# Optimization experiments

Measured on AMD Instinct MI355X. Metric: run time of the kernel, lower is better.

The kernel has to match this reference:

```python
import jax, jax.numpy as jnp
import numpy as np

N, E, DIN, HID, DOUT = 50000, 800000, 128, 128, 64
NEG_SLOPE = 0.2


def setup_inputs() -> dict:
    key = jax.random.key(0)
    ks = jax.random.split(key, 16)
    x = jax.random.normal(ks[0], (N, DIN), dtype=jnp.float32)
    edge_index = jax.random.randint(ks[1], (2, E), 0, N, dtype=jnp.int64)

    def lin(k, fan_in, fan_out):
        kw, kb = jax.random.split(k)
        s = 1.0 / np.sqrt(fan_in)
        W = jax.random.uniform(kw, (fan_in, fan_out), jnp.float32, -s, s)
        b = jax.random.uniform(kb, (fan_out,), jnp.float32, -s, s)
        return W, b

    Wl, bl = lin(ks[2], DIN, DIN)   # GATv2 lin_l
    Wr, br = lin(ks[3], DIN, DIN)   # GATv2 lin_r
    att = jax.random.uniform(ks[4], (DIN,), jnp.float32, -1.0 / np.sqrt(DIN), 1.0 / np.sqrt(DIN))
    bg = jnp.zeros((DIN,), jnp.float32)  # GAT output bias
    W1, b1 = lin(ks[5], DIN, HID)   # ChebConv K=1 -> plain linear
    W2, b2 = lin(ks[6], HID, HID)
    W3, b3 = lin(ks[7], HID, DOUT)
    return {"x": x, "edge_index": edge_index, "Wl": Wl, "bl": bl, "Wr": Wr,
            "br": br, "att": att, "bg": bg, "W1": W1, "b1": b1,
            "W2": W2, "b2": b2, "W3": W3, "b3": b3}


def reference(x, edge_index, Wl, bl, Wr, br, att, bg, W1, b1, W2, b2, W3, b3):
    n = x.shape[0]
    # GATv2Conv adds self loops by default
    loop = jnp.arange(n, dtype=edge_index.dtype)
    src = jnp.concatenate([edge_index[0], loop])  # source j
    dst = jnp.concatenate([edge_index[1], loop])  # target i

    xl = x @ Wl + bl  # [N, DIN]
    xr = x @ Wr + br  # [N, DIN]

    # GATv2 edge scores: leaky_relu(x_l[j] + x_r[i]) . att
    e = jax.nn.leaky_relu(xl[src] + xr[dst], NEG_SLOPE)  # [E+N, DIN]
    a = e @ att                                          # [E+N]

    # softmax over incoming edges of each destination node
    amax = jax.ops.segment_max(a, dst, num_segments=n)
    ea = jnp.exp(a - amax[dst])
    denom = jax.ops.segment_sum(ea, dst, num_segments=n)
    alpha = ea / denom[dst]                              # [E+N]

    # aggregate messages alpha * x_l[j] at destinations
    h = jax.ops.segment_sum(alpha[:, None] * xl[src], dst, num_segments=n) + bg

    # ChebConv with K=1 reduces to a linear layer (T_0(L) = I)
    h = jax.nn.relu(h @ W1 + b1)
    h = jax.nn.relu(h @ W2 + b2)
    # dropout_rate = 0.0 -> identity
    return h @ W3 + b3
```

## Files before the change

kernel.cpp:

```cpp
#include <hip/hip_runtime.h>
#include <hip/hip_bf16.h>

#define DIN 128
#define NEG_SLOPE 0.2f
#define PTILE 2048
#define FCAP 8192
#define CVT_BLKS 289

typedef __attribute__((ext_vector_type(8))) short bf16x8;
typedef __attribute__((ext_vector_type(8))) unsigned short u16x8;
typedef __attribute__((ext_vector_type(4))) float f32x4;
typedef __attribute__((ext_vector_type(2))) float f32x2;
typedef __attribute__((ext_vector_type(4))) unsigned int u32x4;

__device__ __forceinline__ ushort f2bf(float f) {
  unsigned u = __float_as_uint(f);
  u += 0x7FFFu + ((u >> 16) & 1u);
  return (ushort)(u >> 16);
}
__device__ __forceinline__ float bf2f(ushort u) {
  return __uint_as_float((unsigned)u << 16);
}
__device__ __forceinline__ f32x2 bfpair(unsigned u) {
  f32x2 r;
  r.x = __uint_as_float(u << 16);
  r.y = __uint_as_float(u & 0xFFFF0000u);
  return r;
}

__global__ __launch_bounds__(256) void cvt_hist_kernel(
    const float* __restrict__ Wl, const float* __restrict__ Wr,
    const float* __restrict__ W1, const float* __restrict__ W2,
    const float* __restrict__ W3,
    ushort* __restrict__ WlT, ushort* __restrict__ WrT,
    ushort* __restrict__ W1T, ushort* __restrict__ W2T,
    ushort* __restrict__ W3T,
    const int* __restrict__ ei, int* __restrict__ ghist, int E) {
  if (blockIdx.x < CVT_BLKS) {
    int i = blockIdx.x * 256 + threadIdx.x;
    if (i < 16384) {
      int k = i >> 7, c = i & 127; WlT[c * 128 + k] = f2bf(Wl[i]);
    } else if (i < 32768) {
      int j = i - 16384; int k = j >> 7, c = j & 127; WrT[c * 128 + k] = f2bf(Wr[j]);
    } else if (i < 49152) {
      int j = i - 32768; int k = j >> 7, c = j & 127; W1T[c * 128 + k] = f2bf(W1[j]);
    } else if (i < 65536) {
      int j = i - 49152; int k = j >> 7, c = j & 127; W2T[c * 128 + k] = f2bf(W2[j]);
    } else if (i < 73728) {
      int j = i - 65536; int k = j >> 6, c = j & 63; W3T[c * 128 + k] = f2bf(W3[j]);
    }
  } else {
    __shared__ int h[256];
    h[threadIdx.x] = 0;
    __syncthreads();
    int tile = blockIdx.x - CVT_BLKS;
    for (int e = tile * PTILE + threadIdx.x;
         e < min(E, (tile + 1) * PTILE); e += 256)
      atomicAdd(&h[ei[E + e] >> 8], 1);
    __syncthreads();
    if (h[threadIdx.x] > 0) atomicAdd(&ghist[threadIdx.x], h[threadIdx.x]);
  }
}

__global__ __launch_bounds__(256) void scan_small_kernel(
    const int* __restrict__ ghist, int* __restrict__ cum,
    int* __restrict__ cursor) {
  __shared__ int sh[256];
  int tid = threadIdx.x;
  int v = ghist[tid];
  sh[tid] = v;
  __syncthreads();
  for (int d = 1; d < 256; d <<= 1) {
    int t = (tid >= d) ? sh[tid - d] : 0;
    __syncthreads();
    sh[tid] += t;
    __syncthreads();
  }
  int exc = sh[tid] - v;
  cum[tid] = exc;
  cursor[tid] = exc;
  if (tid == 255) cum[256] = sh[255];
}

__global__ __launch_bounds__(256) void lin_partition_kernel(
    const float* __restrict__ x,
    const ushort* __restrict__ WlT, const float* __restrict__ bl,
    const ushort* __restrict__ WrT, const float* __restrict__ br,
    ushort* __restrict__ xl, ushort* __restrict__ xr, int n, int nblk_lin,
    const int* __restrict__ ei, unsigned* __restrict__ part,
    int* __restrict__ cursor, int E) {
  if ((int)blockIdx.x < nblk_lin) {
    const int tid = threadIdx.x;
    const int wv = tid >> 6, lane = tid & 63;
    const int m = lane & 15, quad = lane >> 4;
    const int colbase = (wv & 1) * 64;
    const int nodew = blockIdx.x * 32 + (wv >> 1) * 16;
    int arow = nodew + m; if (arow >= n) arow = n - 1;
    f32x4 accl[4], accr[4];
#pragma unroll
    for (int nt = 0; nt < 4; nt++) { accl[nt] = (f32x4){0,0,0,0}; accr[nt] = (f32x4){0,0,0,0}; }
#pragma unroll
    for (int kk = 0; kk < 4; kk++) {
      int k0 = kk * 32 + quad * 8;
      const float4* xp = (const float4*)(x + (long)arow * 128 + k0);
      float4 x0 = xp[0], x1 = xp[1];
      bf16x8 af;
      af[0] = (short)f2bf(x0.x); af[1] = (short)f2bf(x0.y);
      af[2] = (short)f2bf(x0.z); af[3] = (short)f2bf(x0.w);
      af[4] = (short)f2bf(x1.x); af[5] = (short)f2bf(x1.y);
      af[6] = (short)f2bf(x1.z); af[7] = (short)f2bf(x1.w);
#pragma unroll
      for (int nt = 0; nt < 4; nt++) {
        int brow = colbase + nt * 16 + m;
        bf16x8 bl8 = *(const bf16x8*)(WlT + brow * 128 + k0);
        bf16x8 br8 = *(const bf16x8*)(WrT + brow * 128 + k0);
        accl[nt] = __builtin_amdgcn_mfma_f32_16x16x32_bf16(af, bl8, accl[nt], 0, 0, 0);
        accr[nt] = __builtin_amdgcn_mfma_f32_16x16x32_bf16(af, br8, accr[nt], 0, 0, 0);
      }
    }
#pragma unroll
    for (int nt = 0; nt < 4; nt++) {
      int col = colbase + nt * 16 + m;
      float vbl = bl[col], vbr = br[col];
#pragma unroll
      for (int r = 0; r < 4; r++) {
        int node = nodew + quad * 4 + r;
        if (node < n) {
          xl[(long)node * 128 + col] = f2bf(accl[nt][r] + vbl);
          xr[(long)node * 128 + col] = f2bf(accr[nt][r] + vbr);
        }
      }
    }
  } else {
    __shared__ int hist[256], pref[256], sexcl[256], curs[256], gbase[256];
    __shared__ unsigned buf[PTILE];
    const int tid = threadIdx.x;
    const int tile0 = ((int)blockIdx.x - nblk_lin) * PTILE;
    const int tcount = min(PTILE, E - tile0);
    hist[tid] = 0;
    __syncthreads();
    unsigned pk[PTILE / 256];
    int cnt = 0;
    for (int i = tid; i < tcount; i += 256) {
      int e = tile0 + i;
      int s = ei[e], d = ei[E + e];
      unsigned p = ((unsigned)d << 16) | (unsigned)s;
      pk[cnt++] = p;
      atomicAdd(&hist[d >> 8], 1);
    }
    __syncthreads();
    int v = hist[tid];
    pref[tid] = v;
    __syncthreads();
    for (int d = 1; d < 256; d <<= 1) {
      int t = (tid >= d) ? pref[tid - d] : 0;
      __syncthreads();
      pref[tid] += t;
      __syncthreads();
    }
    int exc = pref[tid] - v;
    sexcl[tid] = exc;
    curs[tid] = exc;
    gbase[tid] = (v > 0) ? atomicAdd(&cursor[tid], v) : 0;
    __syncthreads();
    for (int j = 0; j < cnt; j++) {
      int b = pk[j] >> 24;
      int pos = atomicAdd(&curs[b], 1);
      buf[pos] = pk[j];
    }
    __syncthreads();
    for (int i = tid; i < tcount; i += 256) {
      unsigned p = buf[i];
      int b = p >> 24;
      part[gbase[b] + (i - sexcl[b])] = p;
    }
  }
}

__global__ __launch_bounds__(512) void fine_kernel(
    const unsigned* __restrict__ part, const int* __restrict__ cum,
    int* __restrict__ offsets, ushort* __restrict__ ssrc,
    int N, int E, int nbuck) {
  __shared__ int hist[256], pref[256], curs[256];
  __shared__ unsigned buf[FCAP], buf2[FCAP];
  const int tid = threadIdx.x;
  const int b = blockIdx.x;
  const int seg0 = cum[b];
  const int len = min(cum[b + 1] - seg0, FCAP);
  if (tid < 256) hist[tid] = 0;
  __syncthreads();
  for (int i = tid; i < len; i += 512) {
    unsigned p = part[seg0 + i];
    buf[i] = p;
    atomicAdd(&hist[(p >> 16) & 255], 1);
  }
  __syncthreads();
  int v = (tid < 256) ? hist[tid] : 0;
  if (tid < 256) pref[tid] = v;
  __syncthreads();
  for (int d = 1; d < 256; d <<= 1) {
    int t = (tid >= d && tid < 256) ? pref[tid - d] : 0;
    __syncthreads();
    if (tid < 256) pref[tid] += t;
    __syncthreads();
  }
  if (tid < 256) {
    int exc = pref[tid] - v;
    curs[tid] = exc;
    int node = b * 256 + tid;
    if (node < N) offsets[node] = seg0 + exc;
  }
  if (b == nbuck - 1 && tid == 0) offsets[N] = E;
  __syncthreads();
  for (int i = tid; i < len; i += 512) {
    unsigned p = buf[i];
    int pos = atomicAdd(&curs[(p >> 16) & 255], 1);
    buf2[pos] = p;
  }
  __syncthreads();
  for (int i = tid; i < len; i += 512)
    ssrc[seg0 + i] = (ushort)(buf2[i] & 0xFFFFu);
}

__global__ __launch_bounds__(256) void node_aggr_kernel(
    const ushort* __restrict__ xl, const ushort* __restrict__ xr,
    const float* __restrict__ att, const float* __restrict__ bg,
    const int* __restrict__ offsets, const ushort* __restrict__ ssrc,
    ushort* __restrict__ h, int n) {
  int wave = (int)((blockIdx.x * (long)blockDim.x + threadIdx.x) >> 6);
  int lane = threadIdx.x & 63;
  if (wave >= n) return;
  const int node = wave;
  const int eg = lane >> 4, sl = lane & 15;
  f32x2 av2[4], r2[4], acc2[4];
  {
    const float4* ap = (const float4*)(att + sl * 8);
    float4 a0 = ap[0], a1 = ap[1];
    av2[0] = (f32x2){a0.x, a0.y}; av2[1] = (f32x2){a0.z, a0.w};
    av2[2] = (f32x2){a1.x, a1.y}; av2[3] = (f32x2){a1.z, a1.w};
  }
  const ushort* xls = xl + sl * 8;
  u32x4 rv = *(const u32x4*)(xr + (long)node * 128 + sl * 8);
  u32x4 lv = *(const u32x4*)(xls + (long)node * 128);
  const int beg = offsets[node];
  const int end = offsets[node + 1];

  int ia = beg + 2 * eg;
  bool va = ia < end, vb = ia + 1 < end;
  int sa = va ? (int)ssrc[ia] : node;
  int sb = vb ? (int)ssrc[ia + 1] : node;
  u32x4 uva = *(const u32x4*)(xls + (long)sa * 128);
  u32x4 uvb = *(const u32x4*)(xls + (long)sb * 128);
  int ian = beg + 8 + 2 * eg;
  bool van = ian < end, vbn = ian + 1 < end;
  int san = van ? (int)ssrc[ian] : node;
  int sbn = vbn ? (int)ssrc[ian + 1] : node;

  float denom;
  {
    f32x2 t2 = {0.f, 0.f};
    f32x2 l2[4];
#pragma unroll
    for (int jp = 0; jp < 4; jp++) {
      r2[jp] = bfpair(rv[jp]);
      l2[jp] = bfpair(lv[jp]);
      f32x2 v = l2[jp] + r2[jp];
      t2 += __builtin_elementwise_max(v, NEG_SLOPE * v) * av2[jp];
    }
    float t = t2.x + t2.y;
#pragma unroll
    for (int off = 1; off < 16; off <<= 1) t += __shfl_xor(t, off);
    float es = __expf(t);
    denom = (eg == 0) ? es : 0.f;
#pragma unroll
    for (int jp = 0; jp < 4; jp++)
      acc2[jp] = (eg == 0) ? es * l2[jp] : (f32x2){0.f, 0.f};
  }

  for (int p = beg; p < end; p += 8) {
    u32x4 uvan = *(const u32x4*)(xls + (long)san * 128);
    u32x4 uvbn = *(const u32x4*)(xls + (long)sbn * 128);
    int ia2 = p + 16 + 2 * eg;
    bool va2 = ia2 < end, vb2 = ia2 + 1 < end;
    int sa2 = va2 ? (int)ssrc[ia2] : node;
    int sb2 = vb2 ? (int)ssrc[ia2 + 1] : node;
    f32x2 ua2[4], ub2[4];
    f32x2 ta2 = {0.f, 0.f}, tb2 = {0.f, 0.f};
#pragma unroll
    for (int jp = 0; jp < 4; jp++) {
      ua2[jp] = bfpair(uva[jp]);
      ub2[jp] = bfpair(uvb[jp]);
      f32x2 wa = ua2[jp] + r2[jp];
      f32x2 wb = ub2[jp] + r2[jp];
      ta2 += __builtin_elementwise_max(wa, NEG_SLOPE * wa) * av2[jp];
      tb2 += __builtin_elementwise_max(wb, NEG_SLOPE * wb) * av2[jp];
    }
    float ta = ta2.x + ta2.y, tb = tb2.x + tb2.y;
#pragma unroll
    for (int off = 1; off < 16; off <<= 1) {
      ta += __shfl_xor(ta, off);
      tb += __shfl_xor(tb, off);
    }
    float ea = va ? __expf(ta) : 0.f;
    float eb = vb ? __expf(tb) : 0.f;
    denom += ea + eb;
#pragma unroll
    for (int jp = 0; jp < 4; jp++)
      acc2[jp] += ea * ua2[jp] + eb * ub2[jp];
    uva = uvan; uvb = uvbn;
    va = van;   vb = vbn;
    san = sa2;  sbn = sb2;
    van = va2;  vbn = vb2;
  }
#pragma unroll
  for (int jp = 0; jp < 4; jp++) {
    acc2[jp].x += __shfl_xor(acc2[jp].x, 16);
    acc2[jp].y += __shfl_xor(acc2[jp].y, 16);
    acc2[jp].x += __shfl_xor(acc2[jp].x, 32);
    acc2[jp].y += __shfl_xor(acc2[jp].y, 32);
  }
  denom += __shfl_xor(denom, 16);
  denom += __shfl_xor(denom, 32);
  if (eg == 0) {
    float inv = 1.0f / denom;
    const float4* bp = (const float4*)(bg + sl * 8);
    float4 g0 = bp[0], g1 = bp[1];
    f32x2 gv[4] = {{g0.x, g0.y}, {g0.z, g0.w}, {g1.x, g1.y}, {g1.z, g1.w}};
    u16x8 o;
#pragma unroll
    for (int jp = 0; jp < 4; jp++) {
      f32x2 hv = acc2[jp] * inv + gv[jp];
      o[2 * jp]     = f2bf(hv.x);
      o[2 * jp + 1] = f2bf(hv.y);
    }
    *(u16x8*)(h + (long)node * 128 + sl * 8) = o;
  }
}

#define LDSP 136
__global__ __launch_bounds__(256) void mlp_mfma_kernel(
    const ushort* __restrict__ hb,
    const ushort* __restrict__ W1T, const float* __restrict__ b1,
    const ushort* __restrict__ W2T, const float* __restrict__ b2,
    const ushort* __restrict__ W3T, const float* __restrict__ b3,
    float* __restrict__ out, int n) {
  __shared__ ushort act[32][LDSP];
  const int tid = threadIdx.x;
  const int wv = tid >> 6, lane = tid & 63;
  const int m = lane & 15, quad = lane >> 4;
  const int half = wv & 1, ng = wv >> 1;
  const int colbase = half * 64;
  const int nodew = blockIdx.x * 32 + ng * 16;
  int arow = nodew + m; if (arow >= n) arow = n - 1;
  f32x4 acc[4];
#pragma unroll
  for (int nt = 0; nt < 4; nt++) acc[nt] = (f32x4){0,0,0,0};
#pragma unroll
  for (int kk = 0; kk < 4; kk++) {
    int k0 = kk * 32 + quad * 8;
    bf16x8 af = *(const bf16x8*)(hb + (long)arow * 128 + k0);
#pragma unroll
    for (int nt = 0; nt < 4; nt++) {
      bf16x8 b8 = *(const bf16x8*)(W1T + (colbase + nt * 16 + m) * 128 + k0);
      acc[nt] = __builtin_amdgcn_mfma_f32_16x16x32_bf16(af, b8, acc[nt], 0, 0, 0);
    }
  }
#pragma unroll
  for (int nt = 0; nt < 4; nt++) {
    int col = colbase + nt * 16 + m;
    float b = b1[col];
#pragma unroll
    for (int r = 0; r < 4; r++)
      act[ng * 16 + quad * 4 + r][col] = f2bf(fmaxf(acc[nt][r] + b, 0.f));
  }
  __syncthreads();
#pragma unroll
  for (int nt = 0; nt < 4; nt++) acc[nt] = (f32x4){0,0,0,0};
#pragma unroll
  for (int kk = 0; kk < 4; kk++) {
    int k0 = kk * 32 + quad * 8;
    bf16x8 af = *(const bf16x8*)(&act[ng * 16 + m][k0]);
#pragma unroll
    for (int nt = 0; nt < 4; nt++) {
      bf16x8 b8 = *(const bf16x8*)(W2T + (colbase + nt * 16 + m) * 128 + k0);
      acc[nt] = __builtin_amdgcn_mfma_f32_16x16x32_bf16(af, b8, acc[nt], 0, 0, 0);
    }
  }
  __syncthreads();
#pragma unroll
  for (int nt = 0; nt < 4; nt++) {
    int col = colbase + nt * 16 + m;
    float b = b2[col];
#pragma unroll
    for (int r = 0; r < 4; r++)
      act[ng * 16 + quad * 4 + r][col] = f2bf(fmaxf(acc[nt][r] + b, 0.f));
  }
  __syncthreads();
  f32x4 acc3[2];
#pragma unroll
  for (int nt = 0; nt < 2; nt++) acc3[nt] = (f32x4){0,0,0,0};
#pragma unroll
  for (int kk = 0; kk < 4; kk++) {
    int k0 = kk * 32 + quad * 8;
    bf16x8 af = *(const bf16x8*)(&act[ng * 16 + m][k0]);
#pragma unroll
    for (int nt = 0; nt < 2; nt++) {
      bf16x8 b8 = *(const bf16x8*)(W3T + (half * 32 + nt * 16 + m) * 128 + k0);
      acc3[nt] = __builtin_amdgcn_mfma_f32_16x16x32_bf16(af, b8, acc3[nt], 0, 0, 0);
    }
  }
#pragma unroll
  for (int nt = 0; nt < 2; nt++) {
    int col = half * 32 + nt * 16 + m;
    float b = b3[col];
#pragma unroll
    for (int r = 0; r < 4; r++) {
      int node = nodew + quad * 4 + r;
      if (node < n) out[(long)node * 64 + col] = acc3[nt][r] + b;
    }
  }
}

extern "C" void kernel_launch(void* const* d_in, const int* in_sizes, int n_in,
                              void* d_out, int out_size, void* d_ws, size_t ws_size,
                              hipStream_t stream) {
  const float* x   = (const float*)d_in[0];
  const int*   ei  = (const int*)d_in[1];
  const float* Wl  = (const float*)d_in[2];
  const float* bl  = (const float*)d_in[3];
  const float* Wr  = (const float*)d_in[4];
  const float* br  = (const float*)d_in[5];
  const float* att = (const float*)d_in[6];
  const float* bg  = (const float*)d_in[7];
  const float* W1  = (const float*)d_in[8];
  const float* b1  = (const float*)d_in[9];
  const float* W2  = (const float*)d_in[10];
  const float* b2  = (const float*)d_in[11];
  const float* W3  = (const float*)d_in[12];
  const float* b3  = (const float*)d_in[13];
  float* out = (float*)d_out;

  const int N = in_sizes[0] / DIN;
  const int E = in_sizes[1] / 2;
  const int nbuck = (N + 255) >> 8;

  char* ws = (char*)d_ws;
  size_t off = 0;
  auto alloc = [&](size_t bytes) {
    void* p = ws + off;
    off += (bytes + 255) & ~(size_t)255;
    return p;
  };
  int* ghist     = (int*)alloc(256 * 4);
  int* cum       = (int*)alloc(257 * 4);
  int* cursor    = (int*)alloc(256 * 4);
  int* offsets   = (int*)alloc(((size_t)N + 4) * 4);
  unsigned* part = (unsigned*)alloc((size_t)E * 4);
  ushort* ssrc   = (ushort*)alloc(((size_t)E + 32) * 2);
  ushort* xlb    = (ushort*)alloc((size_t)N * DIN * 2);
  ushort* xrb    = (ushort*)alloc((size_t)N * DIN * 2);
  ushort* hbf    = (ushort*)alloc((size_t)N * DIN * 2);
  ushort* WlT    = (ushort*)alloc(16384 * 2);
  ushort* WrT    = (ushort*)alloc(16384 * 2);
  ushort* W1T    = (ushort*)alloc(16384 * 2);
  ushort* W2T    = (ushort*)alloc(16384 * 2);
  ushort* W3T    = (ushort*)alloc(8192 * 2);
  (void)ws_size;

  hipMemsetAsync(ghist, 0, 256 * 4, stream);

  int ntile = (E + PTILE - 1) / PTILE;
  cvt_hist_kernel<<<CVT_BLKS + ntile, 256, 0, stream>>>(
      Wl, Wr, W1, W2, W3, WlT, WrT, W1T, W2T, W3T, ei, ghist, E);

  scan_small_kernel<<<1, 256, 0, stream>>>(ghist, cum, cursor);

  int nblk32 = (N + 31) / 32;
  lin_partition_kernel<<<nblk32 + ntile, 256, 0, stream>>>(
      x, WlT, bl, WrT, br, xlb, xrb, N, nblk32, ei, part, cursor, E);

  fine_kernel<<<nbuck, 512, 0, stream>>>(part, cum, offsets, ssrc, N, E, nbuck);

  int nwblk = (N + 3) / 4;
  node_aggr_kernel<<<nwblk, 256, 0, stream>>>(xlb, xrb, att, bg,
                                              offsets, ssrc, hbf, N);

  mlp_mfma_kernel<<<nblk32, 256, 0, stream>>>(hbf, W1T, b1, W2T, b2,
                                              W3T, b3, out, N);
}
```

Measured before the change: 248.8 us.

## Stage GEMM A-tiles in LDS, widen fine sort blocks, drop aggr prefetch

The linear and MLP kernels now load each 32-row input tile into LDS once, with coalesced loads, and read MFMA A fragments from shared memory. Before, each wave loaded directly from global memory and the two column-half waves duplicated those loads. The fine bucket-sort kernel moves from 512 to 1024 threads per block. The node aggregation kernel drops its software-pipelined prefetch of the next edges' source indices and rows, which simplifies the loop and lowers register use but exposes gather latency.

```diff
diff --git a/kernel.cpp b/kernel.cpp
--- a/kernel.cpp
+++ b/kernel.cpp
@@ -6,6 +6,7 @@
 #define PTILE 2048
 #define FCAP 8192
 #define CVT_BLKS 289
+#define LDSP 136
 
 typedef __attribute__((ext_vector_type(8))) short bf16x8;
 typedef __attribute__((ext_vector_type(8))) unsigned short u16x8;
@@ -90,32 +91,41 @@
     const int* __restrict__ ei, unsigned* __restrict__ part,
     int* __restrict__ cursor, int E) {
   if ((int)blockIdx.x < nblk_lin) {
+    __shared__ ushort xs[32][LDSP];
     const int tid = threadIdx.x;
+    const int node0 = blockIdx.x * 32;
+    for (int i = tid; i < 1024; i += 256) {
+      int row = i >> 5, c4 = i & 31;
+      int node = node0 + row;
+      float4 v = {0.f, 0.f, 0.f, 0.f};
+      if (node < n) v = ((const float4*)(x + (long)node * 128))[c4];
+      ushort4 o;
+      o.x = f2bf(v.x); o.y = f2bf(v.y); o.z = f2bf(v.z); o.w = f2bf(v.w);
+      *(ushort4*)(&xs[row][c4 * 4]) = o;
+    }
+    __syncthreads();
     const int wv = tid >> 6, lane = tid & 63;
     const int m = lane & 15, quad = lane >> 4;
     const int colbase = (wv & 1) * 64;
-    const int nodew = blockIdx.x * 32 + (wv >> 1) * 16;
-    int arow = nodew + m; if (arow >= n) arow = n - 1;
+    const int ng = wv >> 1;
+    const int nodew = node0 + ng * 16;
+    bf16x8 af[4];
+#pragma unroll
+    for (int kk = 0; kk < 4; kk++)
+      af[kk] = *(const bf16x8*)(&xs[ng * 16 + m][kk * 32 + quad * 8]);
     f32x4 accl[4], accr[4];
 #pragma unroll
     for (int nt = 0; nt < 4; nt++) { accl[nt] = (f32x4){0,0,0,0}; accr[nt] = (f32x4){0,0,0,0}; }
 #pragma unroll
     for (int kk = 0; kk < 4; kk++) {
       int k0 = kk * 32 + quad * 8;
-      const float4* xp = (const float4*)(x + (long)arow * 128 + k0);
-      float4 x0 = xp[0], x1 = xp[1];
-      bf16x8 af;
-      af[0] = (short)f2bf(x0.x); af[1] = (short)f2bf(x0.y);
-      af[2] = (short)f2bf(x0.z); af[3] = (short)f2bf(x0.w);
-      af[4] = (short)f2bf(x1.x); af[5] = (short)f2bf(x1.y);
-      af[6] = (short)f2bf(x1.z); af[7] = (short)f2bf(x1.w);
 #pragma unroll
       for (int nt = 0; nt < 4; nt++) {
         int brow = colbase + nt * 16 + m;
         bf16x8 bl8 = *(const bf16x8*)(WlT + brow * 128 + k0);
         bf16x8 br8 = *(const bf16x8*)(WrT + brow * 128 + k0);
-        accl[nt] = __builtin_amdgcn_mfma_f32_16x16x32_bf16(af, bl8, accl[nt], 0, 0, 0);
-        accr[nt] = __builtin_amdgcn_mfma_f32_16x16x32_bf16(af, br8, accr[nt], 0, 0, 0);
+        accl[nt] = __builtin_amdgcn_mfma_f32_16x16x32_bf16(af[kk], bl8, accl[nt], 0, 0, 0);
+        accr[nt] = __builtin_amdgcn_mfma_f32_16x16x32_bf16(af[kk], br8, accr[nt], 0, 0, 0);
       }
     }
 #pragma unroll
@@ -177,7 +187,7 @@
   }
 }
 
-__global__ __launch_bounds__(512) void fine_kernel(
+__global__ __launch_bounds__(1024) void fine_kernel(
     const unsigned* __restrict__ part, const int* __restrict__ cum,
     int* __restrict__ offsets, ushort* __restrict__ ssrc,
     int N, int E, int nbuck) {
@@ -189,7 +199,7 @@
   const int len = min(cum[b + 1] - seg0, FCAP);
   if (tid < 256) hist[tid] = 0;
   __syncthreads();
-  for (int i = tid; i < len; i += 512) {
+  for (int i = tid; i < len; i += 1024) {
     unsigned p = part[seg0 + i];
     buf[i] = p;
     atomicAdd(&hist[(p >> 16) & 255], 1);
@@ -212,13 +222,13 @@
   }
   if (b == nbuck - 1 && tid == 0) offsets[N] = E;
   __syncthreads();
-  for (int i = tid; i < len; i += 512) {
+  for (int i = tid; i < len; i += 1024) {
     unsigned p = buf[i];
     int pos = atomicAdd(&curs[(p >> 16) & 255], 1);
     buf2[pos] = p;
   }
   __syncthreads();
-  for (int i = tid; i < len; i += 512)
+  for (int i = tid; i < len; i += 1024)
     ssrc[seg0 + i] = (ushort)(buf2[i] & 0xFFFFu);
 }
 
@@ -242,20 +252,6 @@
   const ushort* xls = xl + sl * 8;
   u32x4 rv = *(const u32x4*)(xr + (long)node * 128 + sl * 8);
   u32x4 lv = *(const u32x4*)(xls + (long)node * 128);
-  const int beg = offsets[node];
-  const int end = offsets[node + 1];
-
-  int ia = beg + 2 * eg;
-  bool va = ia < end, vb = ia + 1 < end;
-  int sa = va ? (int)ssrc[ia] : node;
-  int sb = vb ? (int)ssrc[ia + 1] : node;
-  u32x4 uva = *(const u32x4*)(xls + (long)sa * 128);
-  u32x4 uvb = *(const u32x4*)(xls + (long)sb * 128);
-  int ian = beg + 8 + 2 * eg;
-  bool van = ian < end, vbn = ian + 1 < end;
-  int san = van ? (int)ssrc[ian] : node;
-  int sbn = vbn ? (int)ssrc[ian + 1] : node;
-
   float denom;
   {
     f32x2 t2 = {0.f, 0.f};
@@ -276,14 +272,15 @@
     for (int jp = 0; jp < 4; jp++)
       acc2[jp] = (eg == 0) ? es * l2[jp] : (f32x2){0.f, 0.f};
   }
-
+  const int beg = offsets[node];
+  const int end = offsets[node + 1];
   for (int p = beg; p < end; p += 8) {
-    u32x4 uvan = *(const u32x4*)(xls + (long)san * 128);
-    u32x4 uvbn = *(const u32x4*)(xls + (long)sbn * 128);
-    int ia2 = p + 16 + 2 * eg;
-    bool va2 = ia2 < end, vb2 = ia2 + 1 < end;
-    int sa2 = va2 ? (int)ssrc[ia2] : node;
-    int sb2 = vb2 ? (int)ssrc[ia2 + 1] : node;
+    int ia = p + 2 * eg;
+    bool va = ia < end, vb = ia + 1 < end;
+    int sa = va ? (int)ssrc[ia] : node;
+    int sb = vb ? (int)ssrc[ia + 1] : node;
+    u32x4 uva = *(const u32x4*)(xls + (long)sa * 128);
+    u32x4 uvb = *(const u32x4*)(xls + (long)sb * 128);
     f32x2 ua2[4], ub2[4];
     f32x2 ta2 = {0.f, 0.f}, tb2 = {0.f, 0.f};
 #pragma unroll
@@ -307,10 +304,6 @@
 #pragma unroll
     for (int jp = 0; jp < 4; jp++)
       acc2[jp] += ea * ua2[jp] + eb * ub2[jp];
-    uva = uvan; uvb = uvbn;
-    va = van;   vb = vbn;
-    san = sa2;  sbn = sb2;
-    van = va2;  vbn = vb2;
   }
 #pragma unroll
   for (int jp = 0; jp < 4; jp++) {
@@ -337,7 +330,6 @@
   }
 }
 
-#define LDSP 136
 __global__ __launch_bounds__(256) void mlp_mfma_kernel(
     const ushort* __restrict__ hb,
     const ushort* __restrict__ W1T, const float* __restrict__ b1,
@@ -346,25 +338,41 @@
     float* __restrict__ out, int n) {
   __shared__ ushort act[32][LDSP];
   const int tid = threadIdx.x;
+  const int node0 = blockIdx.x * 32;
+  for (int i = tid; i < 512; i += 256) {
+    int row = i >> 4, c8 = i & 15;
+    int node = node0 + row;
+    u16x8 v;
+    if (node < n) v = *(const u16x8*)(hb + (long)node * 128 + c8 * 8);
+    else {
+#pragma unroll
+      for (int j = 0; j < 8; j++) v[j] = 0;
+    }
+    *(u16x8*)(&act[row][c8 * 8]) = v;
+  }
+  __syncthreads();
   const int wv = tid >> 6, lane = tid & 63;
   const int m = lane & 15, quad = lane >> 4;
   const int half = wv & 1, ng = wv >> 1;
   const int colbase = half * 64;
-  const int nodew = blockIdx.x * 32 + ng * 16;
-  int arow = nodew + m; if (arow >= n) arow = n - 1;
+  const int nodew = node0 + ng * 16;
+  bf16x8 af[4];
   f32x4 acc[4];
+#pragma unroll
+  for (int kk = 0; kk < 4; kk++)
+    af[kk] = *(const bf16x8*)(&act[ng * 16 + m][kk * 32 + quad * 8]);
 #pragma unroll
   for (int nt = 0; nt < 4; nt++) acc[nt] = (f32x4){0,0,0,0};
 #pragma unroll
   for (int kk = 0; kk < 4; kk++) {
     int k0 = kk * 32 + quad * 8;
-    bf16x8 af = *(const bf16x8*)(hb + (long)arow * 128 + k0);
 #pragma unroll
     for (int nt = 0; nt < 4; nt++) {
       bf16x8 b8 = *(const bf16x8*)(W1T + (colbase + nt * 16 + m) * 128 + k0);
-      acc[nt] = __builtin_amdgcn_mfma_f32_16x16x32_bf16(af, b8, acc[nt], 0, 0, 0);
-    }
-  }
+      acc[nt] = __builtin_amdgcn_mfma_f32_16x16x32_bf16(af[kk], b8, acc[nt], 0, 0, 0);
+    }
+  }
+  __syncthreads();
 #pragma unroll
   for (int nt = 0; nt < 4; nt++) {
     int col = colbase + nt * 16 + m;
@@ -375,15 +383,17 @@
   }
   __syncthreads();
 #pragma unroll
+  for (int kk = 0; kk < 4; kk++)
+    af[kk] = *(const bf16x8*)(&act[ng * 16 + m][kk * 32 + quad * 8]);
+#pragma unroll
   for (int nt = 0; nt < 4; nt++) acc[nt] = (f32x4){0,0,0,0};
 #pragma unroll
   for (int kk = 0; kk < 4; kk++) {
     int k0 = kk * 32 + quad * 8;
-    bf16x8 af = *(const bf16x8*)(&act[ng * 16 + m][k0]);
 #pragma unroll
     for (int nt = 0; nt < 4; nt++) {
       bf16x8 b8 = *(const bf16x8*)(W2T + (colbase + nt * 16 + m) * 128 + k0);
-      acc[nt] = __builtin_amdgcn_mfma_f32_16x16x32_bf16(af, b8, acc[nt], 0, 0, 0);
+      acc[nt] = __builtin_amdgcn_mfma_f32_16x16x32_bf16(af[kk], b8, acc[nt], 0, 0, 0);
     }
   }
   __syncthreads();
@@ -396,17 +406,19 @@
       act[ng * 16 + quad * 4 + r][col] = f2bf(fmaxf(acc[nt][r] + b, 0.f));
   }
   __syncthreads();
+#pragma unroll
+  for (int kk = 0; kk < 4; kk++)
+    af[kk] = *(const bf16x8*)(&act[ng * 16 + m][kk * 32 + quad * 8]);
   f32x4 acc3[2];
 #pragma unroll
   for (int nt = 0; nt < 2; nt++) acc3[nt] = (f32x4){0,0,0,0};
 #pragma unroll
   for (int kk = 0; kk < 4; kk++) {
     int k0 = kk * 32 + quad * 8;
-    bf16x8 af = *(const bf16x8*)(&act[ng * 16 + m][k0]);
 #pragma unroll
     for (int nt = 0; nt < 2; nt++) {
       bf16x8 b8 = *(const bf16x8*)(W3T + (half * 32 + nt * 16 + m) * 128 + k0);
-      acc3[nt] = __builtin_amdgcn_mfma_f32_16x16x32_bf16(af, b8, acc3[nt], 0, 0, 0);
+      acc3[nt] = __builtin_amdgcn_mfma_f32_16x16x32_bf16(af[kk], b8, acc3[nt], 0, 0, 0);
     }
   }
 #pragma unroll
@@ -479,7 +491,7 @@
   lin_partition_kernel<<<nblk32 + ntile, 256, 0, stream>>>(
       x, WlT, bl, WrT, br, xlb, xrb, N, nblk32, ei, part, cursor, E);
 
-  fine_kernel<<<nbuck, 512, 0, stream>>>(part, cum, offsets, ssrc, N, E, nbuck);
+  fine_kernel<<<nbuck, 1024, 0, stream>>>(part, cum, offsets, ssrc, N, E, nbuck);
 
   int nwblk = (N + 3) / 4;
   node_aggr_kernel<<<nwblk, 256, 0, stream>>>(xlb, xrb, att, bg,
```

Measured after the change: 243.5 us. -2.1%, faster.
